# Kernel optimization log

Measured on AMD Instinct MI355X. Metric: run time of the kernel, lower is better.

The kernel has to match this reference:

```python
import jax, jax.numpy as jnp
import numpy as np

N = 50000      # nodes
E = 320000     # edges
D_NODE = 256   # node feature size
D_EDGE = 128   # raw edge feature size
T_DIM = 64     # time encoder out_channels
H = 8          # heads (auto_num_heads(256) -> 8)
C = 32         # per-head dim = 256 // 8
D_E_IN = D_EDGE + T_DIM  # edge_dim into lin_edge


def setup_inputs() -> dict:
    key = jax.random.key(0)
    ks = jax.random.split(key, 16)
    s_n = 1.0 / np.sqrt(D_NODE)
    s_e = 1.0 / np.sqrt(D_E_IN)
    return {
        "edge_tuples": jax.random.randint(ks[0], (2, E), 0, N, dtype=jnp.int64)
        if jax.config.jax_enable_x64 else jax.random.randint(ks[0], (2, E), 0, N),
        "edge_feats": jax.random.normal(ks[1], (E, D_EDGE), jnp.float32),
        "edge_times_rel": jax.random.uniform(ks[2], (E,), jnp.float32) * 100.0,
        "node_feats": jax.random.normal(ks[3], (N, D_NODE), jnp.float32),
        # time encoder: Linear(1, T_DIM) followed by cos
        "w_time": jax.random.normal(ks[4], (T_DIM,), jnp.float32),
        "b_time": jax.random.normal(ks[5], (T_DIM,), jnp.float32),
        # TransformerConv linears (out = H*C = 256)
        "Wq": jax.random.normal(ks[6], (H * C, D_NODE), jnp.float32) * s_n,
        "bq": jnp.zeros((H * C,), jnp.float32),
        "Wk": jax.random.normal(ks[7], (H * C, D_NODE), jnp.float32) * s_n,
        "bk": jnp.zeros((H * C,), jnp.float32),
        "Wv": jax.random.normal(ks[8], (H * C, D_NODE), jnp.float32) * s_n,
        "bv": jnp.zeros((H * C,), jnp.float32),
        "We": jax.random.normal(ks[9], (H * C, D_E_IN), jnp.float32) * s_e,  # lin_edge, no bias
        "Ws": jax.random.normal(ks[10], (H * C, D_NODE), jnp.float32) * s_n,  # lin_skip
        "bs": jnp.zeros((H * C,), jnp.float32),
    }


def reference(edge_tuples, edge_feats, edge_times_rel, node_feats,
              w_time, b_time, Wq, bq, Wk, bk, Wv, bv, We, Ws, bs):
    n_nodes = node_feats.shape[0]
    n_edges = edge_tuples.shape[1]
    src, dst = edge_tuples[0], edge_tuples[1]

    # TGN time encoder: cos(t * w + b)  -> [E, T_DIM]
    tfeat = jnp.cos(edge_times_rel[:, None] * w_time[None, :] + b_time)
    e_attr = jnp.concatenate([tfeat, edge_feats], axis=1)  # [E, T_DIM + D_EDGE]

    # dense per-node projections, then gather per edge
    q = (node_feats @ Wq.T + bq)[dst].reshape(n_edges, H, C)
    k = (node_feats @ Wk.T + bk)[src].reshape(n_edges, H, C)
    v = (node_feats @ Wv.T + bv)[src].reshape(n_edges, H, C)
    ep = (e_attr @ We.T).reshape(n_edges, H, C)

    k = k + ep
    alpha = jnp.sum(q * k, axis=-1) / jnp.sqrt(jnp.asarray(C, q.dtype))  # [E, H]

    # segment softmax over edges grouped by destination node
    m = jax.ops.segment_max(alpha, dst, num_segments=n_nodes)  # [N, H]
    m = jnp.where(jnp.isfinite(m), m, 0.0)
    ea = jnp.exp(alpha - m[dst])
    denom = jax.ops.segment_sum(ea, dst, num_segments=n_nodes)
    a = ea / (denom[dst] + 1e-16)  # [E, H]

    # weighted scatter-aggregate of (value + edge) messages
    msg = a[:, :, None] * (v + ep)  # [E, H, C]
    out = jax.ops.segment_sum(msg, dst, num_segments=n_nodes).reshape(n_nodes, H * C)

    # root / skip connection
    out = out + node_feats @ Ws.T + bs
    return out
```

## Files before the change

### kernel.cpp

```cpp
#include <hip/hip_runtime.h>
#include <hip/hip_bf16.h>
#include <math.h>

#define NN 50000
#define NE 320000
#define SCAN_NBLK ((NN + 255) / 256)

typedef __attribute__((ext_vector_type(8))) short bf16x8;
typedef __attribute__((ext_vector_type(4))) float floatx4;
typedef __attribute__((ext_vector_type(4))) unsigned int uintx4;

static __device__ __forceinline__ unsigned pack2bf(float a, float b) {
    __hip_bfloat162 h = __float22bfloat162_rn(make_float2(a, b));
    return *reinterpret_cast<unsigned*>(&h);
}
static __device__ __forceinline__ unsigned short f2bf(float x) {
    __hip_bfloat16 h = __float2bfloat16(x);
    return *reinterpret_cast<unsigned short*>(&h);
}
static __device__ __forceinline__ float bf2f(unsigned short u) {
    return __uint_as_float(((unsigned)u) << 16);
}
static __device__ __forceinline__ float bflo(unsigned u) {
    return __uint_as_float(u << 16);
}
static __device__ __forceinline__ float bfhi(unsigned u) {
    return __uint_as_float(u & 0xffff0000u);
}
static __device__ __forceinline__ void gload_lds16(const void* g, void* l) {
    __builtin_amdgcn_global_load_lds(
        (const __attribute__((address_space(1))) void*)g,
        (__attribute__((address_space(3))) void*)l, 16, 0, 0);
}

__global__ __launch_bounds__(256)
void cvt_bf16_kernel(const float* __restrict__ in,
                     unsigned short* __restrict__ out, int n8)
{
    int t = blockIdx.x * 256 + threadIdx.x;
    if (t >= n8) return;
    const float4* p = (const float4*)in + (size_t)t * 2;
    float4 a = p[0], b = p[1];
    uint4 u;
    u.x = pack2bf(a.x, a.y); u.y = pack2bf(a.z, a.w);
    u.z = pack2bf(b.x, b.y); u.w = pack2bf(b.z, b.w);
    ((uint4*)out)[t] = u;
}

__global__ __launch_bounds__(256)
void tf_kernel(const float* __restrict__ tvals,
               const float* __restrict__ w_time,
               const float* __restrict__ b_time,
               unsigned short* __restrict__ eab)
{
    int t = blockIdx.x * 256 + threadIdx.x;
    int e = t >> 3, part = t & 7;
    if (e >= NE) return;
    float tv = tvals[e];
    int k = part * 8;
    float v[8];
    #pragma unroll
    for (int i = 0; i < 8; ++i)
        v[i] = cosf(fmaf(tv, w_time[k + i], b_time[k + i]));
    uint4 u;
    u.x = pack2bf(v[0], v[1]); u.y = pack2bf(v[2], v[3]);
    u.z = pack2bf(v[4], v[5]); u.w = pack2bf(v[6], v[7]);
    *(uint4*)(eab + (size_t)e * 192 + k) = u;
}

__global__ __launch_bounds__(256)
void efcvt_kernel(const float* __restrict__ efeat,
                  unsigned short* __restrict__ eab)
{
    int t = blockIdx.x * 256 + threadIdx.x;
    int e = t >> 4, part = t & 15;
    if (e >= NE) return;
    const float4* p = (const float4*)(efeat + (size_t)e * 128 + part * 8);
    float4 a = p[0], b = p[1];
    uint4 u;
    u.x = pack2bf(a.x, a.y); u.y = pack2bf(a.z, a.w);
    u.z = pack2bf(b.x, b.y); u.w = pack2bf(b.z, b.w);
    *(uint4*)(eab + (size_t)e * 192 + 64 + part * 8) = u;
}

__global__ __launch_bounds__(256)
void node_gemm_kernel(const unsigned short* __restrict__ Xb,
                      const unsigned short* __restrict__ Wqb,
                      const unsigned short* __restrict__ Wkb,
                      const unsigned short* __restrict__ Wvb,
                      const unsigned short* __restrict__ Wsb,
                      const float* __restrict__ bq, const float* __restrict__ bk,
                      const float* __restrict__ bv, const float* __restrict__ bs,
                      unsigned short* __restrict__ qb,
                      unsigned short* __restrict__ kb,
                      unsigned short* __restrict__ vb,
                      float* __restrict__ outS)
{
    const int m0  = blockIdx.x * 128;
    const int ct  = blockIdx.y;
    const int mat = ct >> 1, half = ct & 1;
    const int colbase = half * 128;

    const unsigned short* __restrict__ W;
    const float* __restrict__ bias;
    switch (mat) {
        case 0:  W = Wqb; bias = bq; break;
        case 1:  W = Wkb; bias = bk; break;
        case 2:  W = Wvb; bias = bv; break;
        default: W = Wsb; bias = bs; break;
    }
    W += (size_t)colbase * 256;

    __shared__ __align__(16) unsigned char smem[32768];
    short* sA = (short*)smem;
    short* sB = (short*)(smem + 16384);

    const int tid  = threadIdx.x;
    const int lane = tid & 63;
    const int wave = tid >> 6;
    const int wm   = (wave & 1) * 64;
    const int wn   = (wave >> 1) * 64;
    const int lr   = lane & 15;
    const int lq   = lane >> 4;

    const int srow = tid >> 3;
    const int scol = (tid & 7) * 8;

    floatx4 acc[4][4];
    #pragma unroll
    for (int i = 0; i < 4; ++i)
        #pragma unroll
        for (int j = 0; j < 4; ++j)
            acc[i][j] = (floatx4){0.f, 0.f, 0.f, 0.f};

    for (int k0 = 0; k0 < 256; k0 += 64) {
        #pragma unroll
        for (int p = 0; p < 4; ++p) {
            int arow = m0 + p * 32 + srow;
            if (arow > NN - 1) arow = NN - 1;
            gload_lds16(Xb + (size_t)arow * 256 + k0 + scol,
                        (char*)sA + p * 4096 + wave * 1024);
            gload_lds16(W + (size_t)(p * 32 + srow) * 256 + k0 + scol,
                        (char*)sB + p * 4096 + wave * 1024);
        }
        __syncthreads();

        #pragma unroll
        for (int ks = 0; ks < 2; ++ks) {
            bf16x8 af[4], bfr[4];
            #pragma unroll
            for (int i = 0; i < 4; ++i)
                af[i] = *(const bf16x8*)&sA[(wm + i * 16 + lr) * 64 + ks * 32 + lq * 8];
            #pragma unroll
            for (int j = 0; j < 4; ++j)
                bfr[j] = *(const bf16x8*)&sB[(wn + j * 16 + lr) * 64 + ks * 32 + lq * 8];
            #pragma unroll
            for (int i = 0; i < 4; ++i)
                #pragma unroll
                for (int j = 0; j < 4; ++j)
                    acc[i][j] = __builtin_amdgcn_mfma_f32_16x16x32_bf16(
                        af[i], bfr[j], acc[i][j], 0, 0, 0);
        }
        __syncthreads();
    }

    if (mat < 3) {
        unsigned short* __restrict__ Cb = (mat == 0) ? qb : (mat == 1) ? kb : vb;
        unsigned short* sOut = (unsigned short*)smem;
        for (int ch = 0; ch < 4; ++ch) {
            __syncthreads();
            if ((ch >> 1) == (wave & 1)) {
                int ibase = (ch & 1) * 2;
                #pragma unroll
                for (int ii = 0; ii < 2; ++ii) {
                    int i = ibase + ii;
                    #pragma unroll
                    for (int j = 0; j < 4; ++j) {
                        int col = wn + j * 16 + lr;
                        float bb = bias[colbase + col];
                        #pragma unroll
                        for (int r = 0; r < 4; ++r) {
                            int rowc = ii * 16 + lq * 4 + r;
                            sOut[rowc * 136 + col] = f2bf(acc[i][j][r] + bb);
                        }
                    }
                }
            }
            __syncthreads();
            #pragma unroll
            for (int p = 0; p < 2; ++p) {
                int rowc = p * 16 + (tid >> 4);
                int off  = (tid & 15) * 8;
                int grow = m0 + ch * 32 + rowc;
                if (grow < NN) {
                    uint4 u = *(const uint4*)&sOut[rowc * 136 + off];
                    *(uint4*)&Cb[(size_t)grow * 256 + colbase + off] = u;
                }
            }
        }
    } else {
        float* sOutF = (float*)smem;
        for (int ch = 0; ch < 8; ++ch) {
            __syncthreads();
            if ((ch >> 2) == (wave & 1)) {
                int i = ch & 3;
                #pragma unroll
                for (int j = 0; j < 4; ++j) {
                    int col = wn + j * 16 + lr;
                    float bb = bias[colbase + col];
                    #pragma unroll
                    for (int r = 0; r < 4; ++r) {
                        int rowc = lq * 4 + r;
                        sOutF[rowc * 132 + col] = acc[i][j][r] + bb;
                    }
                }
            }
            __syncthreads();
            #pragma unroll
            for (int p = 0; p < 2; ++p) {
                int rowc = p * 8 + (tid >> 5);
                int off  = (tid & 31) * 4;
                int grow = m0 + ch * 16 + rowc;
                if (grow < NN) {
                    float4 f = *(const float4*)&sOutF[rowc * 132 + off];
                    *(float4*)&outS[(size_t)grow * 256 + colbase + off] = f;
                }
            }
        }
    }
}

__global__ __launch_bounds__(256)
void edge_gemm_kernel(const unsigned short* __restrict__ eab,
                      const unsigned short* __restrict__ Web,
                      unsigned short* __restrict__ epb)
{
    const int m0 = blockIdx.x * 128;
    const int n0 = blockIdx.y * 128;

    __shared__ __align__(16) unsigned char smem[32768];
    short* sA = (short*)smem;
    short* sB = (short*)(smem + 16384);

    const int tid  = threadIdx.x;
    const int lane = tid & 63;
    const int wave = tid >> 6;
    const int wm   = (wave & 1) * 64;
    const int wn   = (wave >> 1) * 64;
    const int lr   = lane & 15;
    const int lq   = lane >> 4;

    const int srow = tid >> 3;
    const int scol = (tid & 7) * 8;

    floatx4 acc[4][4];
    #pragma unroll
    for (int i = 0; i < 4; ++i)
        #pragma unroll
        for (int j = 0; j < 4; ++j)
            acc[i][j] = (floatx4){0.f, 0.f, 0.f, 0.f};

    for (int k0 = 0; k0 < 192; k0 += 64) {
        #pragma unroll
        for (int p = 0; p < 4; ++p) {
            gload_lds16(eab + (size_t)(m0 + p * 32 + srow) * 192 + k0 + scol,
                        (char*)sA + p * 4096 + wave * 1024);
            gload_lds16(Web + (size_t)(n0 + p * 32 + srow) * 192 + k0 + scol,
                        (char*)sB + p * 4096 + wave * 1024);
        }
        __syncthreads();

        #pragma unroll
        for (int ks = 0; ks < 2; ++ks) {
            bf16x8 af[4], bfr[4];
            #pragma unroll
            for (int i = 0; i < 4; ++i)
                af[i] = *(const bf16x8*)&sA[(wm + i * 16 + lr) * 64 + ks * 32 + lq * 8];
            #pragma unroll
            for (int j = 0; j < 4; ++j)
                bfr[j] = *(const bf16x8*)&sB[(wn + j * 16 + lr) * 64 + ks * 32 + lq * 8];
            #pragma unroll
            for (int i = 0; i < 4; ++i)
                #pragma unroll
                for (int j = 0; j < 4; ++j)
                    acc[i][j] = __builtin_amdgcn_mfma_f32_16x16x32_bf16(
                        af[i], bfr[j], acc[i][j], 0, 0, 0);
        }
        __syncthreads();
    }

    unsigned short* sOut = (unsigned short*)smem;
    for (int ch = 0; ch < 4; ++ch) {
        __syncthreads();
        if ((ch >> 1) == (wave & 1)) {
            int ibase = (ch & 1) * 2;
            #pragma unroll
            for (int ii = 0; ii < 2; ++ii) {
                int i = ibase + ii;
                #pragma unroll
                for (int j = 0; j < 4; ++j) {
                    int col = wn + j * 16 + lr;
                    #pragma unroll
                    for (int r = 0; r < 4; ++r) {
                        int rowc = ii * 16 + lq * 4 + r;
                        sOut[rowc * 136 + col] = f2bf(acc[i][j][r]);
                    }
                }
            }
        }
        __syncthreads();
        #pragma unroll
        for (int p = 0; p < 2; ++p) {
            int rowc = p * 16 + (tid >> 4);
            int off  = (tid & 15) * 8;
            int grow = m0 + ch * 32 + rowc;
            uint4 u = *(const uint4*)&sOut[rowc * 136 + off];
            *(uint4*)&epb[(size_t)grow * 256 + n0 + off] = u;
        }
    }
}

__global__ __launch_bounds__(256)
void deg_kernel(const int* __restrict__ et, int* __restrict__ deg)
{
    int e = blockIdx.x * 256 + threadIdx.x;
    if (e < NE) atomicAdd(&deg[et[NE + e]], 1);
}

__global__ __launch_bounds__(256)
void blocksum_kernel(const int* __restrict__ deg, int* __restrict__ bsum)
{
    int idx = blockIdx.x * 256 + threadIdx.x;
    int v = (idx < NN) ? deg[idx] : 0;
    #pragma unroll
    for (int off = 1; off < 64; off <<= 1) v += __shfl_xor(v, off);
    __shared__ int s[4];
    if ((threadIdx.x & 63) == 0) s[threadIdx.x >> 6] = v;
    __syncthreads();
    if (threadIdx.x == 0) bsum[blockIdx.x] = s[0] + s[1] + s[2] + s[3];
}

__global__ __launch_bounds__(256)
void bscan_kernel(int* __restrict__ bsum, int* __restrict__ rowstart)
{
    __shared__ int s[256];
    int t = threadIdx.x;
    int v = (t < SCAN_NBLK) ? bsum[t] : 0;
    s[t] = v;
    __syncthreads();
    #pragma unroll
    for (int off = 1; off < 256; off <<= 1) {
        int u = (t >= off) ? s[t - off] : 0;
        __syncthreads();
        s[t] += u;
        __syncthreads();
    }
    if (t < SCAN_NBLK) bsum[t] = (t == 0) ? 0 : s[t - 1];
    if (t == 0) rowstart[NN] = s[SCAN_NBLK - 1];
}

__global__ __launch_bounds__(256)
void chunkscan_kernel(const int* __restrict__ deg, const int* __restrict__ bsum,
                      int* __restrict__ rowstart, int* __restrict__ cursor)
{
    __shared__ int s[256];
    int t = threadIdx.x;
    int idx = blockIdx.x * 256 + t;
    int v = (idx < NN) ? deg[idx] : 0;
    s[t] = v;
    __syncthreads();
    #pragma unroll
    for (int off = 1; off < 256; off <<= 1) {
        int u = (t >= off) ? s[t - off] : 0;
        __syncthreads();
        s[t] += u;
        __syncthreads();
    }
    if (idx < NN) {
        int ex = bsum[blockIdx.x] + s[t] - v;
        rowstart[idx] = ex;
        cursor[idx]   = ex;
    }
}

__global__ __launch_bounds__(256)
void scatter_kernel(const int* __restrict__ et,
                    int* __restrict__ cursor,
                    int2* __restrict__ eslist)
{
    int e = blockIdx.x * 256 + threadIdx.x;
    if (e < NE) {
        int d   = et[NE + e];
        int pos = atomicAdd(&cursor[d], 1);
        eslist[pos] = make_int2(e, et[e]);
    }
}

static __device__ __forceinline__ void edge_proc(
    uint4 ku, uint4 vu, uintx4 eu, const float* q, float mask,
    float* a, float& accd)
{
    float pe0 = bflo(eu[0]), pe1 = bfhi(eu[0]);
    float pe2 = bflo(eu[1]), pe3 = bfhi(eu[1]);
    float pe4 = bflo(eu[2]), pe5 = bfhi(eu[2]);
    float pe6 = bflo(eu[3]), pe7 = bfhi(eu[3]);

    float part;
    part = q[0] * (bflo(ku.x) + pe0);
    part = fmaf(q[1], bfhi(ku.x) + pe1, part);
    part = fmaf(q[2], bflo(ku.y) + pe2, part);
    part = fmaf(q[3], bfhi(ku.y) + pe3, part);
    part = fmaf(q[4], bflo(ku.z) + pe4, part);
    part = fmaf(q[5], bfhi(ku.z) + pe5, part);
    part = fmaf(q[6], bflo(ku.w) + pe6, part);
    part = fmaf(q[7], bfhi(ku.w) + pe7, part);
    part += __shfl_xor(part, 1);
    part += __shfl_xor(part, 2);

    float ea = __expf(part * 0.17677669529663687f) * mask;

    a[0] = fmaf(ea, bflo(vu.x) + pe0, a[0]);
    a[1] = fmaf(ea, bfhi(vu.x) + pe1, a[1]);
    a[2] = fmaf(ea, bflo(vu.y) + pe2, a[2]);
    a[3] = fmaf(ea, bfhi(vu.y) + pe3, a[3]);
    a[4] = fmaf(ea, bflo(vu.z) + pe4, a[4]);
    a[5] = fmaf(ea, bfhi(vu.z) + pe5, a[5]);
    a[6] = fmaf(ea, bflo(vu.w) + pe6, a[6]);
    a[7] = fmaf(ea, bfhi(vu.w) + pe7, a[7]);
    accd += ea;
}

__global__ __launch_bounds__(256)
void fused_agg_kernel(const int2* __restrict__ eslist,
                      const int* __restrict__ rowstart,
                      const unsigned short* __restrict__ qb,
                      const unsigned short* __restrict__ kb,
                      const unsigned short* __restrict__ vb,
                      const unsigned short* __restrict__ epb,
                      float* __restrict__ out)
{
    const int n = blockIdx.x * 4 + (threadIdx.x >> 6);
    if (n >= NN) return;
    const int lane = threadIdx.x & 63;
    const int half = lane >> 5;
    const int co   = (lane & 31) * 8;

    uint4 qu = *(const uint4*)(qb + (size_t)n * 256 + co);
    float q[8] = { bflo(qu.x), bfhi(qu.x), bflo(qu.y), bfhi(qu.y),
                   bflo(qu.z), bfhi(qu.z), bflo(qu.w), bfhi(qu.w) };

    float a[8] = {0.f, 0.f, 0.f, 0.f, 0.f, 0.f, 0.f, 0.f};
    float accd = 0.f;

    const int s0 = rowstart[n];
    const int s1 = rowstart[n + 1];

    int i = s0;
    for (; i + 4 <= s1; i += 4) {
        const int2 pA = eslist[i + half];
        const int2 pB = eslist[i + 2 + half];
        uint4 kA = *(const uint4*)(kb + (size_t)pA.y * 256 + co);
        uint4 vA = *(const uint4*)(vb + (size_t)pA.y * 256 + co);
        uintx4 eA = __builtin_nontemporal_load(
                        (const uintx4*)(epb + (size_t)pA.x * 256 + co));
        uint4 kB = *(const uint4*)(kb + (size_t)pB.y * 256 + co);
        uint4 vB = *(const uint4*)(vb + (size_t)pB.y * 256 + co);
        uintx4 eB = __builtin_nontemporal_load(
                        (const uintx4*)(epb + (size_t)pB.x * 256 + co));

        edge_proc(kA, vA, eA, q, 1.f, a, accd);
        edge_proc(kB, vB, eB, q, 1.f, a, accd);
    }
    for (; i + 2 <= s1; i += 2) {
        const int2 pA = eslist[i + half];
        uint4 kA = *(const uint4*)(kb + (size_t)pA.y * 256 + co);
        uint4 vA = *(const uint4*)(vb + (size_t)pA.y * 256 + co);
        uintx4 eA = __builtin_nontemporal_load(
                        (const uintx4*)(epb + (size_t)pA.x * 256 + co));
        edge_proc(kA, vA, eA, q, 1.f, a, accd);
    }
    if (i < s1) {
        int idx = i + half;
        float mask = (idx < s1) ? 1.f : 0.f;
        if (idx >= s1) idx = s1 - 1;
        const int2 pA = eslist[idx];
        uint4 kA = *(const uint4*)(kb + (size_t)pA.y * 256 + co);
        uint4 vA = *(const uint4*)(vb + (size_t)pA.y * 256 + co);
        uintx4 eA = __builtin_nontemporal_load(
                        (const uintx4*)(epb + (size_t)pA.x * 256 + co));
        edge_proc(kA, vA, eA, q, mask, a, accd);
    }

    #pragma unroll
    for (int j = 0; j < 8; ++j) a[j] += __shfl_xor(a[j], 32);
    accd += __shfl_xor(accd, 32);

    if (half == 0) {
        const float inv = 1.f / (accd + 1e-16f);
        float* po = out + (size_t)n * 256 + co;
        float4 o0 = ((const float4*)po)[0];
        float4 o1 = ((const float4*)po)[1];
        o0.x = fmaf(a[0], inv, o0.x);
        o0.y = fmaf(a[1], inv, o0.y);
        o0.z = fmaf(a[2], inv, o0.z);
        o0.w = fmaf(a[3], inv, o0.w);
        o1.x = fmaf(a[4], inv, o1.x);
        o1.y = fmaf(a[5], inv, o1.y);
        o1.z = fmaf(a[6], inv, o1.z);
        o1.w = fmaf(a[7], inv, o1.w);
        ((float4*)po)[0] = o0;
        ((float4*)po)[1] = o1;
    }
}

extern "C" void kernel_launch(void* const* d_in, const int* in_sizes, int n_in,
                              void* d_out, int out_size, void* d_ws, size_t ws_size,
                              hipStream_t stream)
{
    const int*   et  = (const int*)  d_in[0];
    const float* ef  = (const float*)d_in[1];
    const float* tv  = (const float*)d_in[2];
    const float* nf  = (const float*)d_in[3];
    const float* w_t = (const float*)d_in[4];
    const float* b_t = (const float*)d_in[5];
    const float* Wq  = (const float*)d_in[6];
    const float* bq  = (const float*)d_in[7];
    const float* Wk  = (const float*)d_in[8];
    const float* bk  = (const float*)d_in[9];
    const float* Wv  = (const float*)d_in[10];
    const float* bv  = (const float*)d_in[11];
    const float* We  = (const float*)d_in[12];
    const float* Ws  = (const float*)d_in[13];
    const float* bs  = (const float*)d_in[14];
    float* out = (float*)d_out;

    unsigned short* qb  = (unsigned short*)d_ws;
    unsigned short* kb  = qb  + (size_t)NN * 256;
    unsigned short* vb  = kb  + (size_t)NN * 256;
    unsigned short* epb = vb  + (size_t)NN * 256;
    unsigned short* nfb = epb + (size_t)NE * 256;
    unsigned short* eab = nfb + (size_t)NN * 256;
    unsigned short* Wqb = eab + (size_t)NE * 192;
    unsigned short* Wkb = Wqb + 65536;
    unsigned short* Wvb = Wkb + 65536;
    unsigned short* Wsb = Wvb + 65536;
    unsigned short* Web = Wsb + 65536;
    int* deg      = (int*)(Web + 49152);
    int* rowstart = deg + NN;
    int* cursor   = rowstart + NN + 1;
    int2* eslist  = (int2*)(cursor + NN);
    int* bsum     = (int*)(eslist + NE);
    size_t need   = (size_t)((char*)(bsum + SCAN_NBLK) - (char*)d_ws);
    if (ws_size < need) return;

    (void)hipMemsetAsync(deg, 0, (size_t)NN * sizeof(int), stream);

    cvt_bf16_kernel<<<(NN * 256 / 8 + 255) / 256, 256, 0, stream>>>(nf, nfb, NN * 256 / 8);
    cvt_bf16_kernel<<<32, 256, 0, stream>>>(Wq, Wqb, 8192);
    cvt_bf16_kernel<<<32, 256, 0, stream>>>(Wk, Wkb, 8192);
    cvt_bf16_kernel<<<32, 256, 0, stream>>>(Wv, Wvb, 8192);
    cvt_bf16_kernel<<<32, 256, 0, stream>>>(Ws, Wsb, 8192);
    cvt_bf16_kernel<<<24, 256, 0, stream>>>(We, Web, 6144);
    tf_kernel<<<(NE * 8 + 255) / 256, 256, 0, stream>>>(tv, w_t, b_t, eab);
    efcvt_kernel<<<(NE * 16 + 255) / 256, 256, 0, stream>>>(ef, eab);

    node_gemm_kernel<<<dim3((NN + 127) / 128, 8), 256, 0, stream>>>(
        nfb, Wqb, Wkb, Wvb, Wsb, bq, bk, bv, bs, qb, kb, vb, out);

    edge_gemm_kernel<<<dim3(NE / 128, 2), 256, 0, stream>>>(eab, Web, epb);

    deg_kernel<<<(NE + 255) / 256, 256, 0, stream>>>(et, deg);
    blocksum_kernel<<<SCAN_NBLK, 256, 0, stream>>>(deg, bsum);
    bscan_kernel<<<1, 256, 0, stream>>>(bsum, rowstart);
    chunkscan_kernel<<<SCAN_NBLK, 256, 0, stream>>>(deg, bsum, rowstart, cursor);
    scatter_kernel<<<(NE + 255) / 256, 256, 0, stream>>>(et, cursor, eslist);

    fused_agg_kernel<<<(NN + 3) / 4, 256, 0, stream>>>(
        eslist, rowstart, qb, kb, vb, epb, out);
}
```

Measured before the change: 640.2 us.

## Fuse time encoding and edge-feature bf16 conversion into edge GEMM A-tile load

Removes the separate tf_kernel and efcvt_kernel that built a bf16 concatenated edge-attribute buffer in global memory. The edge GEMM now computes the cosine time features and converts the raw fp32 edge features to bf16 while filling its shared-memory A tile. This saves the write and re-read of a 320000x192 bf16 intermediate and two launches. The A tile row stride is padded from 64 to 72 elements, which should cut LDS bank conflicts. The cost is that the cosine and conversion work is done twice, because the grid has two column blocks.

Measured after the change: 615.6 us. -3.9%, faster.

```diff
diff --git a/kernel.cpp b/kernel.cpp
--- a/kernel.cpp
+++ b/kernel.cpp
@@ -45,42 +45,6 @@
     u.x = pack2bf(a.x, a.y); u.y = pack2bf(a.z, a.w);
     u.z = pack2bf(b.x, b.y); u.w = pack2bf(b.z, b.w);
     ((uint4*)out)[t] = u;
-}
-
-__global__ __launch_bounds__(256)
-void tf_kernel(const float* __restrict__ tvals,
-               const float* __restrict__ w_time,
-               const float* __restrict__ b_time,
-               unsigned short* __restrict__ eab)
-{
-    int t = blockIdx.x * 256 + threadIdx.x;
-    int e = t >> 3, part = t & 7;
-    if (e >= NE) return;
-    float tv = tvals[e];
-    int k = part * 8;
-    float v[8];
-    #pragma unroll
-    for (int i = 0; i < 8; ++i)
-        v[i] = cosf(fmaf(tv, w_time[k + i], b_time[k + i]));
-    uint4 u;
-    u.x = pack2bf(v[0], v[1]); u.y = pack2bf(v[2], v[3]);
-    u.z = pack2bf(v[4], v[5]); u.w = pack2bf(v[6], v[7]);
-    *(uint4*)(eab + (size_t)e * 192 + k) = u;
-}
-
-__global__ __launch_bounds__(256)
-void efcvt_kernel(const float* __restrict__ efeat,
-                  unsigned short* __restrict__ eab)
-{
-    int t = blockIdx.x * 256 + threadIdx.x;
-    int e = t >> 4, part = t & 15;
-    if (e >= NE) return;
-    const float4* p = (const float4*)(efeat + (size_t)e * 128 + part * 8);
-    float4 a = p[0], b = p[1];
-    uint4 u;
-    u.x = pack2bf(a.x, a.y); u.y = pack2bf(a.z, a.w);
-    u.z = pack2bf(b.x, b.y); u.w = pack2bf(b.z, b.w);
-    *(uint4*)(eab + (size_t)e * 192 + 64 + part * 8) = u;
 }
 
 __global__ __launch_bounds__(256)
@@ -231,16 +195,19 @@
 }
 
 __global__ __launch_bounds__(256)
-void edge_gemm_kernel(const unsigned short* __restrict__ eab,
+void edge_gemm_kernel(const float* __restrict__ tvals,
+                      const float* __restrict__ w_time,
+                      const float* __restrict__ b_time,
+                      const float* __restrict__ ef,
                       const unsigned short* __restrict__ Web,
                       unsigned short* __restrict__ epb)
 {
     const int m0 = blockIdx.x * 128;
     const int n0 = blockIdx.y * 128;
 
-    __shared__ __align__(16) unsigned char smem[32768];
+    __shared__ __align__(16) unsigned char smem[34816];
     short* sA = (short*)smem;
-    short* sB = (short*)(smem + 16384);
+    short* sB = (short*)(smem + 18432);
 
     const int tid  = threadIdx.x;
     const int lane = tid & 63;
@@ -253,6 +220,9 @@
     const int srow = tid >> 3;
     const int scol = (tid & 7) * 8;
 
+    const int arow = tid >> 1;
+    const int ac0  = (tid & 1) * 32;
+
     floatx4 acc[4][4];
     #pragma unroll
     for (int i = 0; i < 4; ++i)
@@ -262,11 +232,35 @@
 
     for (int k0 = 0; k0 < 192; k0 += 64) {
         #pragma unroll
-        for (int p = 0; p < 4; ++p) {
-            gload_lds16(eab + (size_t)(m0 + p * 32 + srow) * 192 + k0 + scol,
-                        (char*)sA + p * 4096 + wave * 1024);
+        for (int p = 0; p < 4; ++p)
             gload_lds16(Web + (size_t)(n0 + p * 32 + srow) * 192 + k0 + scol,
                         (char*)sB + p * 4096 + wave * 1024);
+
+        unsigned pk[16];
+        if (k0 == 0) {
+            float tvv = tvals[m0 + arow];
+            #pragma unroll
+            for (int j = 0; j < 16; ++j) {
+                float a = cosf(fmaf(tvv, w_time[ac0 + 2 * j],     b_time[ac0 + 2 * j]));
+                float b = cosf(fmaf(tvv, w_time[ac0 + 2 * j + 1], b_time[ac0 + 2 * j + 1]));
+                pk[j] = pack2bf(a, b);
+            }
+        } else {
+            const float4* src = (const float4*)(ef + (size_t)(m0 + arow) * 128
+                                                + (k0 - 64) + ac0);
+            #pragma unroll
+            for (int j = 0; j < 8; ++j) {
+                float4 f = src[j];
+                pk[2 * j]     = pack2bf(f.x, f.y);
+                pk[2 * j + 1] = pack2bf(f.z, f.w);
+            }
+        }
+        {
+            uint4* dst = (uint4*)&sA[arow * 72 + ac0];
+            dst[0] = make_uint4(pk[0],  pk[1],  pk[2],  pk[3]);
+            dst[1] = make_uint4(pk[4],  pk[5],  pk[6],  pk[7]);
+            dst[2] = make_uint4(pk[8],  pk[9],  pk[10], pk[11]);
+            dst[3] = make_uint4(pk[12], pk[13], pk[14], pk[15]);
         }
         __syncthreads();
 
@@ -275,7 +269,7 @@
             bf16x8 af[4], bfr[4];
             #pragma unroll
             for (int i = 0; i < 4; ++i)
-                af[i] = *(const bf16x8*)&sA[(wm + i * 16 + lr) * 64 + ks * 32 + lq * 8];
+                af[i] = *(const bf16x8*)&sA[(wm + i * 16 + lr) * 72 + ks * 32 + lq * 8];
             #pragma unroll
             for (int j = 0; j < 4; ++j)
                 bfr[j] = *(const bf16x8*)&sB[(wn + j * 16 + lr) * 64 + ks * 32 + lq * 8];
@@ -539,8 +533,7 @@
     unsigned short* vb  = kb  + (size_t)NN * 256;
     unsigned short* epb = vb  + (size_t)NN * 256;
     unsigned short* nfb = epb + (size_t)NE * 256;
-    unsigned short* eab = nfb + (size_t)NN * 256;
-    unsigned short* Wqb = eab + (size_t)NE * 192;
+    unsigned short* Wqb = nfb + (size_t)NN * 256;
     unsigned short* Wkb = Wqb + 65536;
     unsigned short* Wvb = Wkb + 65536;
     unsigned short* Wsb = Wvb + 65536;
@@ -561,13 +554,12 @@
     cvt_bf16_kernel<<<32, 256, 0, stream>>>(Wv, Wvb, 8192);
     cvt_bf16_kernel<<<32, 256, 0, stream>>>(Ws, Wsb, 8192);
     cvt_bf16_kernel<<<24, 256, 0, stream>>>(We, Web, 6144);
-    tf_kernel<<<(NE * 8 + 255) / 256, 256, 0, stream>>>(tv, w_t, b_t, eab);
-    efcvt_kernel<<<(NE * 16 + 255) / 256, 256, 0, stream>>>(ef, eab);
 
     node_gemm_kernel<<<dim3((NN + 127) / 128, 8), 256, 0, stream>>>(
         nfb, Wqb, Wkb, Wvb, Wsb, bq, bk, bv, bs, qb, kb, vb, out);
 
-    edge_gemm_kernel<<<dim3(NE / 128, 2), 256, 0, stream>>>(eab, Web, epb);
+    edge_gemm_kernel<<<dim3(NE / 128, 2), 256, 0, stream>>>(
+        tv, w_t, b_t, ef, Web, epb);
 
     deg_kernel<<<(NE + 255) / 256, 256, 0, stream>>>(et, deg);
     blocksum_kernel<<<SCAN_NBLK, 256, 0, stream>>>(deg, bsum);
```
